# Kernel optimization log

Measured on AMD Instinct MI355X. Metric: run time of the kernel, lower is better.

Reference implementation:

```python
import jax, jax.numpy as jnp
import numpy as np
from jax.scipy.special import gammaln

DIM = 64
N_FT = 1024
X_RANGE = 0.3
TWO_PI = 2.0 * np.pi


def gaussian_kernel_fun_ft(k, dim, scale_sq):
    # 1D Fourier coefficients of the sliced Gaussian kernel exp(-r^2/(2 sigma^2)):
    # f_hat(k) = pi^{d/2}/Gamma(d/2) * (2 pi sigma^2)^{d/2} * |k|^{d-1} * exp(-2 pi^2 sigma^2 k^2)
    # computed in log-space for stability at large d.
    logk = jnp.log(jnp.maximum(jnp.abs(k), 1e-30))
    log_f = (
        0.5 * dim * jnp.log(jnp.float32(np.pi))
        + 0.5 * dim * jnp.log(TWO_PI * scale_sq)
        - gammaln(jnp.float32(dim / 2.0))
        + (dim - 1) * logk
        - 2.0 * jnp.float32(np.pi**2) * scale_sq * k**2
    )
    return jnp.where(k == 0, jnp.float32(0.0), jnp.exp(log_f))


def setup_inputs() -> dict:
    key = jax.random.key(0)
    k1, k2, k3, k4 = jax.random.split(key, 4)
    N, M, P = 8192, 8192, 16
    return {
        "x": jax.random.normal(k1, (N, DIM), dtype=jnp.float32),
        "y": jax.random.normal(k2, (M, DIM), dtype=jnp.float32),
        "x_weights": jax.random.normal(k3, (N,), dtype=jnp.float32),
        "xis": jax.random.normal(k4, (P, DIM), dtype=jnp.float32),
        "scale": 10,
        "P": P,
    }


def reference(x, y, x_weights, xis, scale, P):
    # rescale all points into the ball of radius x_range (as fastsum_fft does)
    scale_f = jnp.float32(scale)
    max_norm = jnp.maximum(
        jnp.max(jnp.sqrt(jnp.sum(x**2, -1))), jnp.max(jnp.sqrt(jnp.sum(y**2, -1)))
    )
    sf = X_RANGE / max_norm
    xs = x * sf  # (N, d)
    ys = y * sf  # (M, d)
    s = scale_f * sf

    h = jnp.arange(-N_FT // 2, N_FT // 2, dtype=x.dtype)  # (K,) frequencies
    kft = gaussian_kernel_fun_ft(h, DIM, s**2)  # (K,)

    # get_xis: normalize random directions onto the unit sphere
    xis_n = xis / jnp.sqrt(jnp.sum(xis**2, -1, keepdims=True))  # (P, d)

    def body(acc, xi):
        xp = TWO_PI * (xs @ xi)  # (N,) projected source nodes, times 2*pi
        yp = TWO_PI * (ys @ xi)  # (M,)
        # adjoint NDFT: a_k = sum_i w_i e^{2 pi i k x_i}, split into real trig sums
        a_re = kft * (x_weights @ jnp.cos(xp[:, None] * h))  # (K,)
        a_im = kft * (x_weights @ jnp.sin(xp[:, None] * h))  # (K,)
        # forward NDFT at targets, real part of sum_k a_k kft_k e^{-2 pi i k y_j}
        out_p = jnp.cos(yp[:, None] * h) @ a_re + jnp.sin(yp[:, None] * h) @ a_im
        return acc + out_p, None

    acc, _ = jax.lax.scan(body, jnp.zeros(y.shape[0], x.dtype), xis_n)
    return acc / jnp.float32(xis_n.shape[0])  # average over the P slices
```

## Files before the change

kernel.cpp:

```cpp
#include <hip/hip_runtime.h>
#include <math.h>

#define DIM  64
#define PMX  16
#define KMX  16
#define POISON 0xAAAAAAAAu
#define FLAGV  0x5A5A5A5Au

#define WS_CNT0  0
#define WS_FLAG0 32
#define WS_CNT1  64
#define WS_FLAG1 96
#define WS_BMAX  128
#define WS_PART  192

__device__ __forceinline__ float aload(const float* p) {
    return __hip_atomic_load(p, __ATOMIC_RELAXED, __HIP_MEMORY_SCOPE_AGENT);
}
__device__ __forceinline__ void astore(float* p, float v) {
    __hip_atomic_store(p, v, __ATOMIC_RELAXED, __HIP_MEMORY_SCOPE_AGENT);
}

__device__ __forceinline__ void gbar(unsigned* cnt, unsigned* flag, unsigned nb) {
    __syncthreads();
    if (threadIdx.x == 0) {
        asm volatile("s_waitcnt vmcnt(0) lgkmcnt(0)" ::: "memory");
        unsigned old = __hip_atomic_fetch_add(cnt, 1u, __ATOMIC_RELAXED,
                                              __HIP_MEMORY_SCOPE_AGENT);
        if (old == POISON + nb - 1u) {
            __hip_atomic_store(flag, FLAGV, __ATOMIC_RELAXED, __HIP_MEMORY_SCOPE_AGENT);
        } else {
            for (int it = 0; it < (1 << 21); ++it) {
                if (__hip_atomic_load(flag, __ATOMIC_RELAXED,
                                      __HIP_MEMORY_SCOPE_AGENT) == FLAGV) break;
                __builtin_amdgcn_s_sleep(2);
            }
        }
    }
    __syncthreads();
}

__global__ void __launch_bounds__(256) k_main(
    const float* __restrict__ x, const float* __restrict__ y,
    const float* __restrict__ xw, const float* __restrict__ xis,
    const int* __restrict__ scale_raw, float* __restrict__ out,
    float* __restrict__ wsF, int N, int M, int P)
{
    __shared__ __align__(16) float sxi[PMX * DIM];
    __shared__ float sinv[PMX];
    __shared__ float sproj[256 * 17];
    __shared__ float sw[256];
    __shared__ float skft[KMX];
    __shared__ float sa[PMX * KMX * 2];
    __shared__ float s_sf_sh;
    __shared__ int   s_kmax;

    const int tid = threadIdx.x;
    const int bid = blockIdx.x;
    const int NXB = N >> 8, NYB = M >> 8;
    const unsigned NB = (unsigned)(NXB + NYB);
    const bool isx = bid < NXB;
    unsigned* bars = (unsigned*)wsF;

    for (int idx = tid * 4; idx < P * DIM; idx += blockDim.x * 4)
        *(float4*)(sxi + idx) = *(const float4*)(xis + idx);
    __syncthreads();
    if (tid < P) {
        float ss = 0.f;
        for (int d = 0; d < DIM; ++d) { float v = sxi[tid * DIM + d]; ss += v * v; }
        sinv[tid] = 1.0f / sqrtf(ss);
    }
    __syncthreads();

    const float* rbase = isx ? (x + ((size_t)bid * 256 + tid) * DIM)
                             : (y + ((size_t)(bid - NXB) * 256 + tid) * DIM);
    const float4* rowp = (const float4*)rbase;
    float ss = 0.f;
    float acc[PMX];
#pragma unroll
    for (int p = 0; p < PMX; ++p) acc[p] = 0.f;
#pragma unroll
    for (int d4 = 0; d4 < DIM / 4; ++d4) {
        float4 v = rowp[d4];
        ss += v.x * v.x + v.y * v.y + v.z * v.z + v.w * v.w;
#pragma unroll
        for (int p = 0; p < PMX; ++p) {
            float4 w = *(const float4*)(sxi + p * DIM + d4 * 4);
            acc[p] = fmaf(v.x, w.x, fmaf(v.y, w.y, fmaf(v.z, w.z, fmaf(v.w, w.w, acc[p]))));
        }
    }
#pragma unroll
    for (int p = 0; p < PMX; ++p) sproj[tid * 17 + p] = acc[p] * sinv[p];
    float mx = ss;
    for (int off = 32; off; off >>= 1) mx = fmaxf(mx, __shfl_down(mx, off));
    __shared__ float sred[4];
    if ((tid & 63) == 0) sred[tid >> 6] = mx;
    __syncthreads();
    if (tid == 0) {
        float m = fmaxf(fmaxf(sred[0], sred[1]), fmaxf(sred[2], sred[3]));
        astore(wsF + WS_BMAX + bid, m);
    }

    gbar(bars + WS_CNT0, bars + WS_FLAG0, NB);

    float m = (tid < (int)NB) ? aload(wsF + WS_BMAX + tid) : 0.f;
    for (int off = 32; off; off >>= 1) m = fmaxf(m, __shfl_down(m, off));
    if (tid == 0) { s_sf_sh = 0.3f / sqrtf(m); s_kmax = 0; }
    __syncthreads();
    const float sf = s_sf_sh;
    int iv = *scale_raw;
    float scale_f = (iv > -1000000 && iv < 1000000) ? (float)iv : __int_as_float(iv);
    float s2 = (scale_f * sf) * (scale_f * sf);
    if (tid < KMX) {
        int k = tid + 1;
        float kf = (float)k;
        const float C0 = 36.63135635f - 78.09222355f;
        float lf = C0 + 32.0f * logf(6.2831853071795864f * s2) + 63.0f * logf(kf)
                 - 19.739208802178716f * s2 * kf * kf;
        float kft = expf(lf);
        skft[tid] = kft;
        if (kft > 0.f) atomicMax(&s_kmax, k);
    }
    __syncthreads();
    const int kmax = min(s_kmax, KMX);

    if (isx) {
        sw[tid] = xw[bid * 256 + tid];
        __syncthreads();
        const int p = tid & 15, kk = tid >> 4;
        if (kk < kmax) {
            const float c1 = sf * (float)(kk + 1);
            float aRe = 0.f, aIm = 0.f;
            for (int i = 0; i < 256; ++i) {
                float pr = sproj[i * 17 + p];
                float w  = sw[i];
                float r = c1 * pr;
                r -= rintf(r);
                aRe = fmaf(w, __builtin_amdgcn_cosf(r), aRe);
                aIm = fmaf(w, __builtin_amdgcn_sinf(r), aIm);
            }
            float kf = skft[kk];
            int idx = (p * KMX + kk) * 2;
            astore(wsF + WS_PART + (size_t)idx * NXB + bid, aRe * kf);
            astore(wsF + WS_PART + (size_t)(idx + 1) * NXB + bid, aIm * kf);
        }
    }

    gbar(bars + WS_CNT1, bars + WS_FLAG1, NB);

    if (!isx) {
        for (int idx = tid; idx < PMX * KMX * 2; idx += blockDim.x) {
            int kk = (idx >> 1) & (KMX - 1);
            float s = 0.f;
            if (kk < kmax) {
                const float* pb = wsF + WS_PART + (size_t)idx * NXB;
                for (int c = 0; c < NXB; ++c) s += aload(pb + c);
            }
            sa[idx] = s;
        }
        __syncthreads();
        float accO = 0.f;
#pragma unroll
        for (int p = 0; p < PMX; ++p) {
            float bp = sf * sproj[tid * 17 + p];
            const float* ap = sa + p * KMX * 2;
            for (int kk = 0; kk < kmax; ++kk) {
                float r = bp * (float)(kk + 1);
                r -= rintf(r);
                accO = fmaf(__builtin_amdgcn_cosf(r), ap[2 * kk],     accO);
                accO = fmaf(__builtin_amdgcn_sinf(r), ap[2 * kk + 1], accO);
            }
        }
        out[(size_t)(bid - NXB) * 256 + tid] = accO * (2.0f / (float)P);
    }
}

extern "C" void kernel_launch(void* const* d_in, const int* in_sizes, int n_in,
                              void* d_out, int out_size, void* d_ws, size_t ws_size,
                              hipStream_t stream) {
    const float* x   = (const float*)d_in[0];
    const float* y   = (const float*)d_in[1];
    const float* xw  = (const float*)d_in[2];
    const float* xis = (const float*)d_in[3];
    const int* scale_raw = (const int*)d_in[4];
    float* wsF = (float*)d_ws;
    int N = in_sizes[0] / DIM;
    int M = in_sizes[1] / DIM;
    int P = in_sizes[3] / DIM;
    int NB = (N >> 8) + (M >> 8);

    k_main<<<NB, 256, 0, stream>>>(x, y, xw, xis, scale_raw,
                                   (float*)d_out, wsF, N, M, P);
}
```

Measured before the change: 96.07 us.

## Split work into 64-row blocks with four threads per row for more CUs

Cuts rows per block from 256 to 64, so the grid grows from 64 to 256 blocks. Each row's 64-dim projection is now split across four threads and combined with xor shuffles. The partial-sum workspace becomes block-major so y-blocks read contiguous rows with unrolled loads. The output phase uses four threads per target, each covering four slices. The aim is to occupy far more compute units during the serialised trig loops; the cost is more partials for each y-block to reduce (128 instead of 32) and a grid barrier spanning 256 blocks with a shorter spin limit.

```diff
diff --git a/kernel.cpp b/kernel.cpp
--- a/kernel.cpp
+++ b/kernel.cpp
@@ -4,6 +4,7 @@
 #define DIM  64
 #define PMX  16
 #define KMX  16
+#define ROWS 64
 #define POISON 0xAAAAAAAAu
 #define FLAGV  0x5A5A5A5Au
 
@@ -12,7 +13,9 @@
 #define WS_CNT1  64
 #define WS_FLAG1 96
 #define WS_BMAX  128
-#define WS_PART  192
+#define WS_PART  512
+
+#define PROW (PMX * KMX * 2)
 
 __device__ __forceinline__ float aload(const float* p) {
     return __hip_atomic_load(p, __ATOMIC_RELAXED, __HIP_MEMORY_SCOPE_AGENT);
@@ -30,7 +33,7 @@
         if (old == POISON + nb - 1u) {
             __hip_atomic_store(flag, FLAGV, __ATOMIC_RELAXED, __HIP_MEMORY_SCOPE_AGENT);
         } else {
-            for (int it = 0; it < (1 << 21); ++it) {
+            for (int it = 0; it < (1 << 19); ++it) {
                 if (__hip_atomic_load(flag, __ATOMIC_RELAXED,
                                       __HIP_MEMORY_SCOPE_AGENT) == FLAGV) break;
                 __builtin_amdgcn_s_sleep(2);
@@ -48,16 +51,17 @@
 {
     __shared__ __align__(16) float sxi[PMX * DIM];
     __shared__ float sinv[PMX];
-    __shared__ float sproj[256 * 17];
-    __shared__ float sw[256];
+    __shared__ float sproj[ROWS * 17];
+    __shared__ float sw[ROWS];
     __shared__ float skft[KMX];
-    __shared__ float sa[PMX * KMX * 2];
+    __shared__ float sa[PMX * 34];
+    __shared__ float sred[4];
     __shared__ float s_sf_sh;
     __shared__ int   s_kmax;
 
     const int tid = threadIdx.x;
     const int bid = blockIdx.x;
-    const int NXB = N >> 8, NYB = M >> 8;
+    const int NXB = N >> 6, NYB = M >> 6;
     const unsigned NB = (unsigned)(NXB + NYB);
     const bool isx = bid < NXB;
     unsigned* bars = (unsigned*)wsF;
@@ -66,34 +70,41 @@
         *(float4*)(sxi + idx) = *(const float4*)(xis + idx);
     __syncthreads();
     if (tid < P) {
-        float ss = 0.f;
-        for (int d = 0; d < DIM; ++d) { float v = sxi[tid * DIM + d]; ss += v * v; }
-        sinv[tid] = 1.0f / sqrtf(ss);
-    }
-    __syncthreads();
-
-    const float* rbase = isx ? (x + ((size_t)bid * 256 + tid) * DIM)
-                             : (y + ((size_t)(bid - NXB) * 256 + tid) * DIM);
+        float ssn = 0.f;
+        for (int d = 0; d < DIM; ++d) { float v = sxi[tid * DIM + d]; ssn += v * v; }
+        sinv[tid] = 1.0f / sqrtf(ssn);
+    }
+    __syncthreads();
+
+    const int row = tid >> 2, q = tid & 3;
+    const float* rbase = (isx ? x + ((size_t)bid * ROWS + row) * DIM
+                              : y + ((size_t)(bid - NXB) * ROWS + row) * DIM) + q * 16;
     const float4* rowp = (const float4*)rbase;
     float ss = 0.f;
     float acc[PMX];
 #pragma unroll
     for (int p = 0; p < PMX; ++p) acc[p] = 0.f;
 #pragma unroll
-    for (int d4 = 0; d4 < DIM / 4; ++d4) {
+    for (int d4 = 0; d4 < 4; ++d4) {
         float4 v = rowp[d4];
         ss += v.x * v.x + v.y * v.y + v.z * v.z + v.w * v.w;
 #pragma unroll
         for (int p = 0; p < PMX; ++p) {
-            float4 w = *(const float4*)(sxi + p * DIM + d4 * 4);
+            const float4 w = *(const float4*)(sxi + p * DIM + q * 16 + d4 * 4);
             acc[p] = fmaf(v.x, w.x, fmaf(v.y, w.y, fmaf(v.z, w.z, fmaf(v.w, w.w, acc[p]))));
         }
     }
-#pragma unroll
-    for (int p = 0; p < PMX; ++p) sproj[tid * 17 + p] = acc[p] * sinv[p];
+    ss += __shfl_xor(ss, 1);
+    ss += __shfl_xor(ss, 2);
+#pragma unroll
+    for (int p = 0; p < PMX; ++p) {
+        float a = acc[p];
+        a += __shfl_xor(a, 1);
+        a += __shfl_xor(a, 2);
+        if (q == 0) sproj[row * 17 + p] = a * sinv[p];
+    }
     float mx = ss;
     for (int off = 32; off; off >>= 1) mx = fmaxf(mx, __shfl_down(mx, off));
-    __shared__ float sred[4];
     if ((tid & 63) == 0) sred[tid >> 6] = mx;
     __syncthreads();
     if (tid == 0) {
@@ -105,7 +116,13 @@
 
     float m = (tid < (int)NB) ? aload(wsF + WS_BMAX + tid) : 0.f;
     for (int off = 32; off; off >>= 1) m = fmaxf(m, __shfl_down(m, off));
-    if (tid == 0) { s_sf_sh = 0.3f / sqrtf(m); s_kmax = 0; }
+    if ((tid & 63) == 0) sred[tid >> 6] = m;
+    __syncthreads();
+    if (tid == 0) {
+        float mm = fmaxf(fmaxf(sred[0], sred[1]), fmaxf(sred[2], sred[3]));
+        s_sf_sh = 0.3f / sqrtf(mm);
+        s_kmax = 0;
+    }
     __syncthreads();
     const float sf = s_sf_sh;
     int iv = *scale_raw;
@@ -125,13 +142,14 @@
     const int kmax = min(s_kmax, KMX);
 
     if (isx) {
-        sw[tid] = xw[bid * 256 + tid];
+        if (tid < ROWS) sw[tid] = xw[bid * ROWS + tid];
         __syncthreads();
         const int p = tid & 15, kk = tid >> 4;
         if (kk < kmax) {
             const float c1 = sf * (float)(kk + 1);
             float aRe = 0.f, aIm = 0.f;
-            for (int i = 0; i < 256; ++i) {
+#pragma unroll 4
+            for (int i = 0; i < ROWS; ++i) {
                 float pr = sproj[i * 17 + p];
                 float w  = sw[i];
                 float r = c1 * pr;
@@ -141,29 +159,43 @@
             }
             float kf = skft[kk];
             int idx = (p * KMX + kk) * 2;
-            astore(wsF + WS_PART + (size_t)idx * NXB + bid, aRe * kf);
-            astore(wsF + WS_PART + (size_t)(idx + 1) * NXB + bid, aIm * kf);
+            float* pb = wsF + WS_PART + (size_t)bid * PROW;
+            astore(pb + idx,     aRe * kf);
+            astore(pb + idx + 1, aIm * kf);
         }
     }
 
     gbar(bars + WS_CNT1, bars + WS_FLAG1, NB);
 
     if (!isx) {
-        for (int idx = tid; idx < PMX * KMX * 2; idx += blockDim.x) {
-            int kk = (idx >> 1) & (KMX - 1);
-            float s = 0.f;
-            if (kk < kmax) {
-                const float* pb = wsF + WS_PART + (size_t)idx * NXB;
-                for (int c = 0; c < NXB; ++c) s += aload(pb + c);
-            }
-            sa[idx] = s;
-        }
+        const int i0 = tid, i1 = tid + 256;
+        const bool act = (((tid >> 1) & 15) < kmax);
+        float s0 = 0.f, s1 = 0.f;
+        const float* base = wsF + WS_PART;
+        for (int c0 = 0; c0 < NXB; c0 += 16) {
+            float v0[16], v1[16];
+            if (act) {
+#pragma unroll
+                for (int u = 0; u < 16; ++u)
+                    v0[u] = aload(base + (size_t)(c0 + u) * PROW + i0);
+#pragma unroll
+                for (int u = 0; u < 16; ++u)
+                    v1[u] = aload(base + (size_t)(c0 + u) * PROW + i1);
+#pragma unroll
+                for (int u = 0; u < 16; ++u) { s0 += v0[u]; s1 += v1[u]; }
+            }
+        }
+        sa[(i0 >> 5) * 34 + (i0 & 31)] = s0;
+        sa[(i1 >> 5) * 34 + (i1 & 31)] = s1;
         __syncthreads();
+
+        const int tgt = tid >> 2, pq = tid & 3;
         float accO = 0.f;
 #pragma unroll
-        for (int p = 0; p < PMX; ++p) {
-            float bp = sf * sproj[tid * 17 + p];
-            const float* ap = sa + p * KMX * 2;
+        for (int pp = 0; pp < 4; ++pp) {
+            const int p = pq * 4 + pp;
+            const float bp = sf * sproj[tgt * 17 + p];
+            const float* ap = sa + p * 34;
             for (int kk = 0; kk < kmax; ++kk) {
                 float r = bp * (float)(kk + 1);
                 r -= rintf(r);
@@ -171,7 +203,9 @@
                 accO = fmaf(__builtin_amdgcn_sinf(r), ap[2 * kk + 1], accO);
             }
         }
-        out[(size_t)(bid - NXB) * 256 + tid] = accO * (2.0f / (float)P);
+        accO += __shfl_xor(accO, 1);
+        accO += __shfl_xor(accO, 2);
+        if (pq == 0) out[(size_t)(bid - NXB) * ROWS + tgt] = accO * (2.0f / (float)P);
     }
 }
 
@@ -187,7 +221,7 @@
     int N = in_sizes[0] / DIM;
     int M = in_sizes[1] / DIM;
     int P = in_sizes[3] / DIM;
-    int NB = (N >> 8) + (M >> 8);
+    int NB = (N >> 6) + (M >> 6);
 
     k_main<<<NB, 256, 0, stream>>>(x, y, xw, xis, scale_raw,
                                    (float*)d_out, wsF, N, M, P);
```

Result: faster. 82.95 us (-13.7%).
